# Performance work log

Hardware: AMD Instinct MI355X
Metric: run time of the kernel (lower is better)

The kernel has to match this reference:

```python
import jax, jax.numpy as jnp
import numpy as np

N_NODES = 50000
N_EDGES = 800000
N_REL = 3
N_GRAPHS = 500
EMB = 128
IN_DIM = EMB * 3
HID = 256
N_CLASS = 10
N_SHAPE, N_COLOR, MAX_POS = 8, 8, 128


def rgcn_layer(h, src, dst, etype, W, root, b):
    """PyG RGCNConv with default aggr='mean':
    out[v] = sum_r mean_{(j->v) in E_r} h[j] @ W[r] + h[v] @ root + b
    Aggregate raw features per (dst, relation) bucket, then apply relation matmuls.
    """
    N, R = h.shape[0], W.shape[0]
    seg = dst * R + etype  # combined (node, relation) segment id
    sums = jax.ops.segment_sum(h[src], seg, num_segments=N * R)          # (N*R, d)
    cnt = jax.ops.segment_sum(jnp.ones(seg.shape, h.dtype), seg, num_segments=N * R)
    mean = (sums / jnp.maximum(cnt, 1.0)[:, None]).reshape(N, R, -1)     # (N, R, d)
    return jnp.einsum('nrd,rdh->nh', mean, W) + h @ root + b


def setup_inputs() -> dict:
    key = jax.random.key(0)
    ks = jax.random.split(key, 20)
    f32 = jnp.float32
    inp = {
        's': jax.random.randint(ks[0], (N_NODES,), 0, N_SHAPE),
        'c': jax.random.randint(ks[1], (N_NODES,), 0, N_COLOR),
        'p': jax.random.randint(ks[2], (N_NODES,), 0, MAX_POS),
        'edge_index': jax.random.randint(ks[3], (2, N_EDGES), 0, N_NODES),
        'edge_type': jax.random.randint(ks[4], (N_EDGES,), 0, N_REL),
        'batch': jnp.sort(jax.random.randint(ks[5], (N_NODES,), 0, N_GRAPHS)),
        'shape_emb': jax.random.normal(ks[6], (N_SHAPE, EMB), f32),
        'color_emb': jax.random.normal(ks[7], (N_COLOR, EMB), f32),
        'pos_emb': jax.random.normal(ks[8], (MAX_POS, EMB), f32),
        'W1': jax.random.normal(ks[9], (N_REL, IN_DIM, HID), f32) / np.sqrt(IN_DIM),
        'root1': jax.random.normal(ks[10], (IN_DIM, HID), f32) / np.sqrt(IN_DIM),
        'b1': jnp.zeros((HID,), f32),
        'W2': jax.random.normal(ks[11], (N_REL, HID, HID), f32) / np.sqrt(HID),
        'root2': jax.random.normal(ks[12], (HID, HID), f32) / np.sqrt(HID),
        'b2': jnp.zeros((HID,), f32),
        'lin_w': jax.random.normal(ks[13], (HID, N_CLASS), f32) / np.sqrt(HID),
        'lin_b': jnp.zeros((N_CLASS,), f32),
    }
    return inp


def reference(s, c, p, edge_index, edge_type, batch,
              shape_emb, color_emb, pos_emb,
              W1, root1, b1, W2, root2, b2, lin_w, lin_b):
    src, dst = edge_index[0], edge_index[1]
    h = jnp.concatenate([shape_emb[s], color_emb[c], pos_emb[p]], axis=-1)  # (N, 3*emb)
    h = jax.nn.relu(rgcn_layer(h, src, dst, edge_type, W1, root1, b1))
    h = jax.nn.relu(rgcn_layer(h, src, dst, edge_type, W2, root2, b2))
    # global_mean_pool over graphs
    gsum = jax.ops.segment_sum(h, batch, num_segments=N_GRAPHS)
    gcnt = jax.ops.segment_sum(jnp.ones((h.shape[0],), h.dtype), batch, num_segments=N_GRAPHS)
    pooled = gsum / jnp.maximum(gcnt, 1.0)[:, None]
    return pooled @ lin_w + lin_b
```

## Files before the change

### kernel.cpp

```cpp
#include <hip/hip_runtime.h>
#include <hip/hip_bf16.h>

#define NN 50000
#define NE 800000
#define NR 3
#define NG 500
#define NB (NN * NR)
#define NCLS 10
#define NCMB 8192
#define CHUNK 2048
#define NBLK ((NB + CHUNK - 1) / CHUNK)

typedef __hip_bfloat16 bf16;
typedef __attribute__((ext_vector_type(8))) short short8;
typedef __attribute__((ext_vector_type(4))) float floatx4;

static __device__ __forceinline__ float b2f(bf16 x) { return __bfloat162float(x); }
static __device__ __forceinline__ bf16  f2b(float x) { return __float2bfloat16(x); }
static __device__ __forceinline__ float bs2f(short x) {
    return __bfloat162float(*reinterpret_cast<const bf16*>(&x));
}
static __device__ __forceinline__ short f2bs(float x) {
    bf16 b = __float2bfloat16(x);
    return *reinterpret_cast<const short*>(&b);
}

__global__ __launch_bounds__(256) void zero_u32(unsigned* __restrict__ p, long n) {
    long i = (long)blockIdx.x * 256 + threadIdx.x;
    if (i < n) p[i] = 0u;
}

__global__ __launch_bounds__(256) void count_edges(const int* __restrict__ ei,
                                                   const int* __restrict__ et,
                                                   int* __restrict__ cnt) {
    int e = blockIdx.x * 256 + threadIdx.x;
    if (e >= NE) return;
    atomicAdd(&cnt[ei[NE + e] * NR + et[e]], 1);
}

__global__ __launch_bounds__(256) void scan_block_sums(const int* __restrict__ cnt,
                                                       int* __restrict__ bsum) {
    __shared__ int sm[256];
    int b = blockIdx.x, t = threadIdx.x;
    int base = b * CHUNK + t * 8, s = 0;
#pragma unroll
    for (int j = 0; j < 8; ++j) { int i = base + j; if (i < NB) s += cnt[i]; }
    sm[t] = s; __syncthreads();
    for (int st = 128; st; st >>= 1) { if (t < st) sm[t] += sm[t + st]; __syncthreads(); }
    if (!t) bsum[b] = sm[0];
}

__global__ void scan_base(const int* __restrict__ bsum, int* __restrict__ bbase,
                          int* __restrict__ off) {
    if (threadIdx.x == 0 && blockIdx.x == 0) {
        int run = 0;
        for (int i = 0; i < NBLK; ++i) { bbase[i] = run; run += bsum[i]; }
        off[NB] = run;
    }
}

__global__ __launch_bounds__(256) void scan_write(const int* __restrict__ cnt,
                                                  const int* __restrict__ bbase,
                                                  int* __restrict__ off,
                                                  int* __restrict__ cursor) {
    int b = blockIdx.x, t = threadIdx.x;
    int base = b * CHUNK + t * 8;
    int v[8], ts = 0;
#pragma unroll
    for (int j = 0; j < 8; ++j) { int i = base + j; v[j] = (i < NB) ? cnt[i] : 0; ts += v[j]; }
    int lane = t & 63, wv = t >> 6;
    int incl = ts;
    for (int d = 1; d < 64; d <<= 1) {
        int o = __shfl_up(incl, d, 64);
        if (lane >= d) incl += o;
    }
    __shared__ int wsum[4];
    if (lane == 63) wsum[wv] = incl;
    __syncthreads();
    int wbase = 0;
    for (int w = 0; w < wv; ++w) wbase += wsum[w];
    int run = bbase[b] + wbase + incl - ts;
#pragma unroll
    for (int j = 0; j < 8; ++j) {
        int i = base + j;
        if (i < NB) { off[i] = run; cursor[i] = run; }
        run += v[j];
    }
}

__global__ __launch_bounds__(256) void scatter_edges(const int* __restrict__ ei,
                                                     const int* __restrict__ et,
                                                     const int* __restrict__ combo,
                                                     int* __restrict__ cursor,
                                                     int* __restrict__ eidx,
                                                     int* __restrict__ ecmb) {
    int e = blockIdx.x * 256 + threadIdx.x;
    if (e >= NE) return;
    int b = ei[NE + e] * NR + et[e];
    int pos = atomicAdd(&cursor[b], 1);
    int s = ei[e];
    eidx[pos] = s;
    ecmb[pos] = combo[s];
}

__global__ __launch_bounds__(256) void tab_gemm(const float* __restrict__ se,
                                                const float* __restrict__ ce,
                                                const float* __restrict__ pe,
                                                const float* __restrict__ W1,
                                                const float* __restrict__ root1,
                                                float* __restrict__ tab) {
    int bid = blockIdx.x;
    int r = bid / 144, row = bid % 144;
    int t = threadIdx.x;
    const float* A; int segk;
    if (row < 8)       { A = se + row * 128;        segk = 0; }
    else if (row < 16) { A = ce + (row - 8) * 128;  segk = 128; }
    else               { A = pe + (row - 16) * 128; segk = 256; }
    const float* W = (r < 3) ? (W1 + (size_t)r * 384 * 256) : root1;
    float acc = 0.f;
    for (int k = 0; k < 128; ++k)
        acc += A[k] * W[(size_t)(segk + k) * 256 + t];
    tab[((size_t)r * 144 + row) * 256 + t] = acc;
}

__global__ __launch_bounds__(256) void node_combo(const int* __restrict__ s,
                                                  const int* __restrict__ c,
                                                  const int* __restrict__ p,
                                                  int* __restrict__ combo) {
    int n = blockIdx.x * 256 + threadIdx.x;
    if (n < NN) combo[n] = (s[n] << 10) | (c[n] << 7) | p[n];
}

__global__ __launch_bounds__(256) void comb_build(const float* __restrict__ tab,
                                                  const float* __restrict__ b1,
                                                  bf16* __restrict__ comb) {
    int bid = blockIdx.x;
    int r = bid >> 13, cmb = bid & (NCMB - 1);
    int d = threadIdx.x;
    int si = cmb >> 10, ci = (cmb >> 7) & 7, pi = cmb & 127;
    const float* tr = tab + (size_t)r * 144 * 256;
    float v = tr[si * 256 + d] + tr[(8 + ci) * 256 + d] + tr[(16 + pi) * 256 + d];
    if (r == 3) v += b1[d];
    comb[(size_t)bid * 256 + d] = f2b(v);
}

__global__ __launch_bounds__(256) void l1_fused(const int* __restrict__ off,
                                                const int* __restrict__ ecmb,
                                                const int* __restrict__ combo,
                                                const bf16* __restrict__ comb,
                                                bf16* __restrict__ h1) {
    int wave = threadIdx.x >> 6, lane = threadIdx.x & 63;
    int dst = blockIdx.x * 4 + wave;
    if (dst >= NN) return;
    int half = lane >> 5, li8 = (lane & 31) * 8;
    float acc[8];
    if (half == 0) {
        int cmbD = combo[dst];
        short8 rv = *(const short8*)(comb + ((size_t)(3 * NCMB) + cmbD) * 256 + li8);
#pragma unroll
        for (int i = 0; i < 8; ++i) acc[i] = bs2f(rv[i]);
    } else {
#pragma unroll
        for (int i = 0; i < 8; ++i) acc[i] = 0.f;
    }
    for (int r = 0; r < NR; ++r) {
        int lo = off[dst * NR + r], hi = off[dst * NR + r + 1];
        if (hi <= lo) continue;
        const bf16* cr = comb + (size_t)r * NCMB * 256;
        float s[8] = {};
        int j = lo;
        for (; j + 8 <= hi; j += 8) {
            int c0 = ecmb[j + half],     c1 = ecmb[j + 2 + half];
            int c2 = ecmb[j + 4 + half], c3 = ecmb[j + 6 + half];
            short8 v0 = *(const short8*)(cr + (size_t)c0 * 256 + li8);
            short8 v1 = *(const short8*)(cr + (size_t)c1 * 256 + li8);
            short8 v2 = *(const short8*)(cr + (size_t)c2 * 256 + li8);
            short8 v3 = *(const short8*)(cr + (size_t)c3 * 256 + li8);
#pragma unroll
            for (int i = 0; i < 8; ++i)
                s[i] += (bs2f(v0[i]) + bs2f(v1[i])) + (bs2f(v2[i]) + bs2f(v3[i]));
        }
        for (; j + 2 <= hi; j += 2) {
            int c0 = ecmb[j + half];
            short8 v0 = *(const short8*)(cr + (size_t)c0 * 256 + li8);
#pragma unroll
            for (int i = 0; i < 8; ++i) s[i] += bs2f(v0[i]);
        }
        if (j < hi && half == 0) {
            short8 v0 = *(const short8*)(cr + (size_t)ecmb[j] * 256 + li8);
#pragma unroll
            for (int i = 0; i < 8; ++i) s[i] += bs2f(v0[i]);
        }
        float inv = 1.0f / (float)(hi - lo);
#pragma unroll
        for (int i = 0; i < 8; ++i) {
            float tot = s[i] + __shfl_xor(s[i], 32);
            if (half == 0) acc[i] += tot * inv;
        }
    }
    if (half == 0) {
        short8 o;
#pragma unroll
        for (int i = 0; i < 8; ++i) o[i] = f2bs(fmaxf(acc[i], 0.f));
        *(short8*)(h1 + (size_t)dst * 256 + li8) = o;
    }
}

__global__ __launch_bounds__(256) void agg_all(const int* __restrict__ off,
                                               const int* __restrict__ eidx,
                                               const bf16* __restrict__ h1,
                                               bf16* __restrict__ hagg) {
    int wave = threadIdx.x >> 6, lane = threadIdx.x & 63;
    int dst = blockIdx.x * 4 + wave;
    if (dst >= NN) return;
    int half = lane >> 5, li8 = (lane & 31) * 8;
    for (int r = 0; r < NR; ++r) {
        int lo = off[dst * NR + r], hi = off[dst * NR + r + 1];
        float s[8] = {};
        int j = lo;
        for (; j + 8 <= hi; j += 8) {
            int e0 = eidx[j + half],     e1 = eidx[j + 2 + half];
            int e2 = eidx[j + 4 + half], e3 = eidx[j + 6 + half];
            short8 v0 = *(const short8*)(h1 + (size_t)e0 * 256 + li8);
            short8 v1 = *(const short8*)(h1 + (size_t)e1 * 256 + li8);
            short8 v2 = *(const short8*)(h1 + (size_t)e2 * 256 + li8);
            short8 v3 = *(const short8*)(h1 + (size_t)e3 * 256 + li8);
#pragma unroll
            for (int i = 0; i < 8; ++i)
                s[i] += (bs2f(v0[i]) + bs2f(v1[i])) + (bs2f(v2[i]) + bs2f(v3[i]));
        }
        for (; j + 2 <= hi; j += 2) {
            int e0 = eidx[j + half];
            short8 v0 = *(const short8*)(h1 + (size_t)e0 * 256 + li8);
#pragma unroll
            for (int i = 0; i < 8; ++i) s[i] += bs2f(v0[i]);
        }
        if (j < hi && half == 0) {
            short8 v0 = *(const short8*)(h1 + (size_t)eidx[j] * 256 + li8);
#pragma unroll
            for (int i = 0; i < 8; ++i) s[i] += bs2f(v0[i]);
        }
        float inv = (hi > lo) ? 1.0f / (float)(hi - lo) : 0.f;
        short8 o;
#pragma unroll
        for (int i = 0; i < 8; ++i) {
            float tot = s[i] + __shfl_xor(s[i], 32);
            o[i] = f2bs(tot * inv);
        }
        if (half == 0)
            *(short8*)(hagg + (size_t)dst * 768 + r * 256 + li8) = o;
    }
}

__global__ __launch_bounds__(256) void conv_w2cat(const float* __restrict__ W2,
                                                  const float* __restrict__ root2,
                                                  bf16* __restrict__ Wt) {
    int idx = blockIdx.x * 256 + threadIdx.x;
    if (idx >= 256 * 1024) return;
    int n = idx >> 10, k = idx & 1023;
    float v = (k < 768) ? W2[((size_t)(k >> 8) * 256 + (k & 255)) * 256 + n]
                        : root2[(size_t)(k - 768) * 256 + n];
    Wt[idx] = f2b(v);
}

__global__ __launch_bounds__(256) void gemm_cat(const bf16* __restrict__ hagg,
                                                const bf16* __restrict__ h1,
                                                const bf16* __restrict__ Wt,
                                                const float* __restrict__ bias,
                                                bf16* __restrict__ h2) {
    __shared__ short As[2][64 * 40];
    __shared__ short Bs[2][128 * 40];
    const int t = threadIdx.x;
    const int wave = t >> 6, lane = t & 63;
    const int quad = lane >> 4, l16 = lane & 15;
    const int mq = (wave & 1) * 32;
    const int nq = (wave >> 1) * 64;
    const int row0 = blockIdx.y * 64, col0 = blockIdx.x * 128;
    const int sr = t >> 2;
    const int sp = (t & 3) * 8;
    const int gmA = row0 + sr;

    auto loadA = [&](int k0) -> short8 {
        short8 v = {};
        int k = k0 + sp;
        if (gmA < NN)
            v = (k < 768) ? *(const short8*)(hagg + (size_t)gmA * 768 + k)
                          : *(const short8*)(h1 + (size_t)gmA * 256 + (k - 768));
        return v;
    };
    auto loadB = [&](int k0, int rlocal) -> short8 {
        return *(const short8*)(Wt + (size_t)(col0 + rlocal) * 1024 + k0 + sp);
    };

    floatx4 acc[2][4] = {};
    short8 ra[3], rb0[3], rb1[3];

#pragma unroll
    for (int s = 0; s < 3; ++s) {
        ra[s] = loadA(s * 32); rb0[s] = loadB(s * 32, sr); rb1[s] = loadB(s * 32, sr + 64);
    }
    *(short8*)&As[0][sr * 40 + sp] = ra[0];
    *(short8*)&Bs[0][sr * 40 + sp] = rb0[0];
    *(short8*)&Bs[0][(sr + 64) * 40 + sp] = rb1[0];
    __syncthreads();

#pragma unroll
    for (int i = 0; i < 32; ++i) {
        const int cur = i & 1, alt = 1 - cur;
        const int fs = i % 3;
        if (i + 3 < 32) {
            int k0 = (i + 3) * 32;
            ra[fs] = loadA(k0); rb0[fs] = loadB(k0, sr); rb1[fs] = loadB(k0, sr + 64);
        }
        short8 af[2], bfr[4];
#pragma unroll
        for (int mi = 0; mi < 2; ++mi)
            af[mi] = *(const short8*)&As[cur][(mq + mi * 16 + l16) * 40 + quad * 8];
#pragma unroll
        for (int ni = 0; ni < 4; ++ni)
            bfr[ni] = *(const short8*)&Bs[cur][(nq + ni * 16 + l16) * 40 + quad * 8];
#pragma unroll
        for (int mi = 0; mi < 2; ++mi)
#pragma unroll
            for (int ni = 0; ni < 4; ++ni)
                acc[mi][ni] = __builtin_amdgcn_mfma_f32_16x16x32_bf16(
                    af[mi], bfr[ni], acc[mi][ni], 0, 0, 0);
        if (i + 1 < 32) {
            const int ws = (i + 1) % 3;
            *(short8*)&As[alt][sr * 40 + sp] = ra[ws];
            *(short8*)&Bs[alt][sr * 40 + sp] = rb0[ws];
            *(short8*)&Bs[alt][(sr + 64) * 40 + sp] = rb1[ws];
        }
        __syncthreads();
    }

#pragma unroll
    for (int mi = 0; mi < 2; ++mi) {
#pragma unroll
        for (int ni = 0; ni < 4; ++ni) {
            int n = col0 + nq + ni * 16 + l16;
            float bn = bias[n];
#pragma unroll
            for (int ii = 0; ii < 4; ++ii) {
                int gm = row0 + mq + mi * 16 + quad * 4 + ii;
                if (gm < NN) {
                    float v = acc[mi][ni][ii] + bn;
                    h2[(size_t)gm * 256 + n] = f2b(fmaxf(v, 0.f));
                }
            }
        }
    }
}

#define PN 64
__global__ __launch_bounds__(256) void pool_rle(const int* __restrict__ batch,
                                                const bf16* __restrict__ H,
                                                float* __restrict__ pool,
                                                float* __restrict__ gcnt) {
    int t = threadIdx.x;
    int n0 = blockIdx.x * PN;
    int nend = n0 + PN; if (nend > NN) nend = NN;
    int curg = batch[n0];
    float acc = 0.f, cnt = 0.f;
    for (int n = n0; n < nend; ++n) {
        int g = batch[n];
        if (g != curg) {
            atomicAdd(&pool[(size_t)curg * 256 + t], acc);
            if (t == 0) atomicAdd(&gcnt[curg], cnt);
            acc = 0.f; cnt = 0.f; curg = g;
        }
        acc += b2f(H[(size_t)n * 256 + t]);
        cnt += 1.f;
    }
    atomicAdd(&pool[(size_t)curg * 256 + t], acc);
    if (t == 0) atomicAdd(&gcnt[curg], cnt);
}

__global__ __launch_bounds__(256) void final_head(const float* __restrict__ pool,
                                                  const float* __restrict__ gcnt,
                                                  const float* __restrict__ lin_w,
                                                  const float* __restrict__ lin_b,
                                                  float* __restrict__ out) {
    __shared__ float sm[256];
    int g = blockIdx.x, t = threadIdx.x;
    float inv = 1.0f / fmaxf(gcnt[g], 1.0f);
    sm[t] = pool[(size_t)g * 256 + t] * inv;
    __syncthreads();
    if (t < NCLS) {
        float s = lin_b[t];
        for (int d = 0; d < 256; ++d) s += sm[d] * lin_w[d * NCLS + t];
        out[g * NCLS + t] = s;
    }
}

extern "C" void kernel_launch(void* const* d_in, const int* in_sizes, int n_in,
                              void* d_out, int out_size, void* d_ws, size_t ws_size,
                              hipStream_t stream) {
    const int*   s_idx = (const int*)d_in[0];
    const int*   c_idx = (const int*)d_in[1];
    const int*   p_idx = (const int*)d_in[2];
    const int*   ei    = (const int*)d_in[3];
    const int*   et    = (const int*)d_in[4];
    const int*   batch = (const int*)d_in[5];
    const float* se    = (const float*)d_in[6];
    const float* ce    = (const float*)d_in[7];
    const float* pe    = (const float*)d_in[8];
    const float* W1    = (const float*)d_in[9];
    const float* root1 = (const float*)d_in[10];
    const float* b1    = (const float*)d_in[11];
    const float* W2    = (const float*)d_in[12];
    const float* root2 = (const float*)d_in[13];
    const float* b2    = (const float*)d_in[14];
    const float* lin_w = (const float*)d_in[15];
    const float* lin_b = (const float*)d_in[16];
    float* out = (float*)d_out;

    char* w = (char*)d_ws;
    size_t o = 0;
    auto alloc = [&](size_t bytes) -> void* {
        o = (o + 15) & ~(size_t)15;
        void* ptr = w + o;
        o += bytes;
        return ptr;
    };
    bf16*  hagg   = (bf16*) alloc((size_t)NN * 768 * 2);
    bf16*  h1     = (bf16*) alloc((size_t)NN * 256 * 2);
    bf16*  h2     = (bf16*) alloc((size_t)NN * 256 * 2);
    bf16*  comb   = (bf16*) alloc((size_t)4 * NCMB * 256 * 2);
    int*   combo  = (int*)  alloc((size_t)NN * 4);
    int*   eidx   = (int*)  alloc((size_t)NE * 4);
    int*   ecmb   = (int*)  alloc((size_t)NE * 4);
    int*   cnt    = (int*)  alloc((size_t)NB * 4);
    int*   off    = (int*)  alloc((size_t)(NB + 1) * 4);
    int*   cursor = (int*)  alloc((size_t)NB * 4);
    int*   bsum   = (int*)  alloc((size_t)NBLK * 4);
    int*   bbase  = (int*)  alloc((size_t)NBLK * 4);
    float* tab    = (float*)alloc((size_t)4 * 144 * 256 * 4);
    bf16*  W2t    = (bf16*) alloc((size_t)256 * 1024 * 2);
    float* pool   = (float*)alloc((size_t)NG * 256 * 4);
    float* gcnt   = (float*)alloc((size_t)NG * 4);
    (void)ws_size;

    node_combo<<<(NN + 255) / 256, 256, 0, stream>>>(s_idx, c_idx, p_idx, combo);
    zero_u32<<<(NB + 255) / 256, 256, 0, stream>>>((unsigned*)cnt, NB);
    count_edges<<<(NE + 255) / 256, 256, 0, stream>>>(ei, et, cnt);
    scan_block_sums<<<NBLK, 256, 0, stream>>>(cnt, bsum);
    scan_base<<<1, 64, 0, stream>>>(bsum, bbase, off);
    scan_write<<<NBLK, 256, 0, stream>>>(cnt, bbase, off, cursor);
    scatter_edges<<<(NE + 255) / 256, 256, 0, stream>>>(ei, et, combo, cursor, eidx, ecmb);

    tab_gemm<<<4 * 144, 256, 0, stream>>>(se, ce, pe, W1, root1, tab);
    comb_build<<<4 * NCMB, 256, 0, stream>>>(tab, b1, comb);
    conv_w2cat<<<(256 * 1024 + 255) / 256, 256, 0, stream>>>(W2, root2, W2t);

    l1_fused<<<(NN + 3) / 4, 256, 0, stream>>>(off, ecmb, combo, comb, h1);

    agg_all<<<(NN + 3) / 4, 256, 0, stream>>>(off, eidx, h1, hagg);
    dim3 g2(2, (NN + 63) / 64);
    gemm_cat<<<g2, 256, 0, stream>>>(hagg, h1, W2t, b2, h2);

    zero_u32<<<(NG * 256 + NG + 255) / 256, 256, 0, stream>>>((unsigned*)pool, NG * 256 + NG);
    pool_rle<<<(NN + PN - 1) / PN, 256, 0, stream>>>(batch, h2, pool, gcnt);
    final_head<<<NG, 256, 0, stream>>>(pool, gcnt, lin_w, lin_b, out);
}
```

Baseline: 439.3 us.

## Pre-swizzle W2 into MFMA fragment layout and drop shared B tile

The concatenated W2/root2 weight is now written in MFMA fragment order, so each lane loads its B operands directly from global memory as coalesced short8 reads, with no pass through shared memory. Each wave gets its own private LDS slab for its 32-row A tile, which removes the block-wide __syncthreads per K step. The aim is to cut LDS traffic and barrier stalls in the layer-2 GEMM. In exchange, B is reloaded from global/L2 by every wave instead of being shared, and prefetch depth drops from three stages to one.

```diff
diff --git a/kernel.cpp b/kernel.cpp
--- a/kernel.cpp
+++ b/kernel.cpp
@@ -254,95 +254,87 @@
 
 __global__ __launch_bounds__(256) void conv_w2cat(const float* __restrict__ W2,
                                                   const float* __restrict__ root2,
-                                                  bf16* __restrict__ Wt) {
+                                                  bf16* __restrict__ Wf) {
     int idx = blockIdx.x * 256 + threadIdx.x;
     if (idx >= 256 * 1024) return;
-    int n = idx >> 10, k = idx & 1023;
-    float v = (k < 768) ? W2[((size_t)(k >> 8) * 256 + (k & 255)) * 256 + n]
-                        : root2[(size_t)(k - 768) * 256 + n];
-    Wt[idx] = f2b(v);
+    int j     = idx & 7;
+    int lane  = (idx >> 3) & 63;
+    int ni    = (idx >> 9) & 3;
+    int chunk = (idx >> 11) & 31;
+    int colblk = idx >> 16;
+    int col = colblk * 64 + ni * 16 + (lane & 15);
+    int k   = chunk * 32 + (lane >> 4) * 8 + j;
+    float v = (k < 768) ? W2[((size_t)(k >> 8) * 256 + (k & 255)) * 256 + col]
+                        : root2[(size_t)(k - 768) * 256 + col];
+    Wf[idx] = f2b(v);
 }
 
 __global__ __launch_bounds__(256) void gemm_cat(const bf16* __restrict__ hagg,
                                                 const bf16* __restrict__ h1,
-                                                const bf16* __restrict__ Wt,
+                                                const bf16* __restrict__ Wf,
                                                 const float* __restrict__ bias,
                                                 bf16* __restrict__ h2) {
-    __shared__ short As[2][64 * 40];
-    __shared__ short Bs[2][128 * 40];
+    __shared__ short lds[4][32 * 40];
     const int t = threadIdx.x;
     const int wave = t >> 6, lane = t & 63;
     const int quad = lane >> 4, l16 = lane & 15;
-    const int mq = (wave & 1) * 32;
-    const int nq = (wave >> 1) * 64;
-    const int row0 = blockIdx.y * 64, col0 = blockIdx.x * 128;
-    const int sr = t >> 2;
-    const int sp = (t & 3) * 8;
-    const int gmA = row0 + sr;
-
-    auto loadA = [&](int k0) -> short8 {
-        short8 v = {};
-        int k = k0 + sp;
-        if (gmA < NN)
-            v = (k < 768) ? *(const short8*)(hagg + (size_t)gmA * 768 + k)
-                          : *(const short8*)(h1 + (size_t)gmA * 256 + (k - 768));
-        return v;
+    const int row0 = blockIdx.y * 64 + (wave & 1) * 32;
+    const int colblk = blockIdx.x * 2 + (wave >> 1);
+    const int rsub = lane >> 2;
+    const int ksub = (lane & 3) * 8;
+    short* A = lds[wave];
+
+    const int r0 = min(row0 + rsub, NN - 1);
+    const int r1 = min(row0 + 16 + rsub, NN - 1);
+    const bf16* gA0 = hagg + (size_t)r0 * 768 + ksub;
+    const bf16* gA1 = hagg + (size_t)r1 * 768 + ksub;
+    const bf16* gH0 = h1 + (size_t)r0 * 256 + ksub;
+    const bf16* gH1 = h1 + (size_t)r1 * 256 + ksub;
+    const short8* bbase = (const short8*)Wf + (size_t)colblk * 32 * 4 * 64 + lane;
+
+    auto loadA2 = [&](int k0, short8& a0, short8& a1) {
+        if (k0 < 768) { a0 = *(const short8*)(gA0 + k0); a1 = *(const short8*)(gA1 + k0); }
+        else          { a0 = *(const short8*)(gH0 + k0 - 768); a1 = *(const short8*)(gH1 + k0 - 768); }
     };
-    auto loadB = [&](int k0, int rlocal) -> short8 {
-        return *(const short8*)(Wt + (size_t)(col0 + rlocal) * 1024 + k0 + sp);
+    auto loadB = [&](int chunk, short8* bf4) {
+        const short8* bp = bbase + (size_t)chunk * 4 * 64;
+#pragma unroll
+        for (int ni = 0; ni < 4; ++ni) bf4[ni] = bp[ni * 64];
     };
 
     floatx4 acc[2][4] = {};
-    short8 ra[3], rb0[3], rb1[3];
-
-#pragma unroll
-    for (int s = 0; s < 3; ++s) {
-        ra[s] = loadA(s * 32); rb0[s] = loadB(s * 32, sr); rb1[s] = loadB(s * 32, sr + 64);
-    }
-    *(short8*)&As[0][sr * 40 + sp] = ra[0];
-    *(short8*)&Bs[0][sr * 40 + sp] = rb0[0];
-    *(short8*)&Bs[0][(sr + 64) * 40 + sp] = rb1[0];
-    __syncthreads();
-
-#pragma unroll
+    short8 aC0, aC1, bC[4], aN0, aN1, bN[4];
+    loadA2(0, aC0, aC1);
+    loadB(0, bC);
+
     for (int i = 0; i < 32; ++i) {
-        const int cur = i & 1, alt = 1 - cur;
-        const int fs = i % 3;
-        if (i + 3 < 32) {
-            int k0 = (i + 3) * 32;
-            ra[fs] = loadA(k0); rb0[fs] = loadB(k0, sr); rb1[fs] = loadB(k0, sr + 64);
-        }
-        short8 af[2], bfr[4];
-#pragma unroll
-        for (int mi = 0; mi < 2; ++mi)
-            af[mi] = *(const short8*)&As[cur][(mq + mi * 16 + l16) * 40 + quad * 8];
-#pragma unroll
-        for (int ni = 0; ni < 4; ++ni)
-            bfr[ni] = *(const short8*)&Bs[cur][(nq + ni * 16 + l16) * 40 + quad * 8];
-#pragma unroll
-        for (int mi = 0; mi < 2; ++mi)
-#pragma unroll
-            for (int ni = 0; ni < 4; ++ni)
-                acc[mi][ni] = __builtin_amdgcn_mfma_f32_16x16x32_bf16(
-                    af[mi], bfr[ni], acc[mi][ni], 0, 0, 0);
+        *(short8*)&A[rsub * 40 + ksub] = aC0;
+        *(short8*)&A[(16 + rsub) * 40 + ksub] = aC1;
         if (i + 1 < 32) {
-            const int ws = (i + 1) % 3;
-            *(short8*)&As[alt][sr * 40 + sp] = ra[ws];
-            *(short8*)&Bs[alt][sr * 40 + sp] = rb0[ws];
-            *(short8*)&Bs[alt][(sr + 64) * 40 + sp] = rb1[ws];
-        }
-        __syncthreads();
+            loadA2((i + 1) * 32, aN0, aN1);
+            loadB(i + 1, bN);
+        }
+        short8 af0 = *(const short8*)&A[l16 * 40 + quad * 8];
+        short8 af1 = *(const short8*)&A[(16 + l16) * 40 + quad * 8];
+#pragma unroll
+        for (int ni = 0; ni < 4; ++ni) {
+            acc[0][ni] = __builtin_amdgcn_mfma_f32_16x16x32_bf16(af0, bC[ni], acc[0][ni], 0, 0, 0);
+            acc[1][ni] = __builtin_amdgcn_mfma_f32_16x16x32_bf16(af1, bC[ni], acc[1][ni], 0, 0, 0);
+        }
+        aC0 = aN0; aC1 = aN1;
+#pragma unroll
+        for (int ni = 0; ni < 4; ++ni) bC[ni] = bN[ni];
     }
 
 #pragma unroll
     for (int mi = 0; mi < 2; ++mi) {
 #pragma unroll
         for (int ni = 0; ni < 4; ++ni) {
-            int n = col0 + nq + ni * 16 + l16;
+            int n = colblk * 64 + ni * 16 + l16;
             float bn = bias[n];
 #pragma unroll
             for (int ii = 0; ii < 4; ++ii) {
-                int gm = row0 + mq + mi * 16 + quad * 4 + ii;
+                int gm = row0 + mi * 16 + quad * 4 + ii;
                 if (gm < NN) {
                     float v = acc[mi][ni][ii] + bn;
                     h2[(size_t)gm * 256 + n] = f2b(fmaxf(v, 0.f));
@@ -436,7 +428,7 @@
     int*   bsum   = (int*)  alloc((size_t)NBLK * 4);
     int*   bbase  = (int*)  alloc((size_t)NBLK * 4);
     float* tab    = (float*)alloc((size_t)4 * 144 * 256 * 4);
-    bf16*  W2t    = (bf16*) alloc((size_t)256 * 1024 * 2);
+    bf16*  Wf     = (bf16*) alloc((size_t)256 * 1024 * 2);
     float* pool   = (float*)alloc((size_t)NG * 256 * 4);
     float* gcnt   = (float*)alloc((size_t)NG * 4);
     (void)ws_size;
@@ -451,13 +443,13 @@
 
     tab_gemm<<<4 * 144, 256, 0, stream>>>(se, ce, pe, W1, root1, tab);
     comb_build<<<4 * NCMB, 256, 0, stream>>>(tab, b1, comb);
-    conv_w2cat<<<(256 * 1024 + 255) / 256, 256, 0, stream>>>(W2, root2, W2t);
+    conv_w2cat<<<(256 * 1024 + 255) / 256, 256, 0, stream>>>(W2, root2, Wf);
 
     l1_fused<<<(NN + 3) / 4, 256, 0, stream>>>(off, ecmb, combo, comb, h1);
 
     agg_all<<<(NN + 3) / 4, 256, 0, stream>>>(off, eidx, h1, hagg);
     dim3 g2(2, (NN + 63) / 64);
-    gemm_cat<<<g2, 256, 0, stream>>>(hagg, h1, W2t, b2, h2);
+    gemm_cat<<<g2, 256, 0, stream>>>(hagg, h1, Wf, b2, h2);
 
     zero_u32<<<(NG * 256 + NG + 255) / 256, 256, 0, stream>>>((unsigned*)pool, NG * 256 + NG);
     pool_rle<<<(NN + PN - 1) / PN, 256, 0, stream>>>(batch, h2, pool, gcnt);
```

Measured after the change: 434.9 us. Within noise of the previous version (-1.0%).
